# Performance work log

Measured on AMD Instinct MI355X. Metric: run time of the kernel, lower is better.

The kernel has to match this reference:

```python
import jax, jax.numpy as jnp
import numpy as np

B, S, D = 32, 512, 512      # batch, seq, feature
E, H, O, K = 8, 2048, 512, 2  # experts, expert hidden, expert out, top_k


def setup_inputs() -> dict:
    key = jax.random.key(0)
    ks = jax.random.split(key, 5)
    sc = lambda k, shape, scale: jax.random.normal(k, shape, jnp.float32) * scale
    return {
        "x": sc(ks[0], (B, S, D), 1.0),
        "attn_w": sc(ks[1], (D, 1), 0.05),
        "attn_b": jnp.zeros((1,), jnp.float32),
        "gate_w": sc(ks[2], (D, E), 0.05),
        "gate_b": jnp.zeros((E,), jnp.float32),
        "w1": sc(ks[3], (E, D, H), 0.02),
        "b1": jnp.zeros((E, H), jnp.float32),
        "w2": sc(ks[4], (E, H, O), 0.02),
        "b2": jnp.zeros((E, O), jnp.float32),
    }


def reference(x, attn_w, attn_b, gate_w, gate_b, w1, b1, w2, b2):
    # --- attention pooling over the sequence axis ---
    scores = x @ attn_w + attn_b                      # [B,S,1]
    aw = jax.nn.softmax(scores, axis=1)               # softmax over seq
    pooled = jnp.sum(x * aw, axis=1)                  # [B,D]

    # --- gating: softmax -> top-k mask -> renormalize ---
    gates = jax.nn.softmax(pooled @ gate_w + gate_b, axis=-1)  # [B,E]
    _, idx = jax.lax.top_k(gates, K)                  # [B,K]
    mask = jnp.sum(jax.nn.one_hot(idx, E, dtype=gates.dtype), axis=-2)  # [B,E]
    g = gates * mask
    g = g / (jnp.sum(g, axis=-1, keepdims=True) + 1e-9)        # [B,E]

    # --- dense all-experts compute (exact GELU, as keras Dense('gelu')) ---
    h = jax.nn.gelu(jnp.einsum('bsd,edh->ebsh', x, w1) + b1[:, None, None, :],
                    approximate=False)                 # [E,B,S,H]
    eo = jax.nn.gelu(jnp.einsum('ebsh,eho->ebso', h, w2) + b2[:, None, None, :],
                     approximate=False)                # [E,B,S,O]

    # --- weighted combine over experts ---
    return jnp.einsum('ebso,be->bso', eo, g)           # [B,S,O]
```

## Files before the change

kernel.cpp:

```cpp
#include <hip/hip_runtime.h>
#include <hip/hip_bf16.h>
#include <math.h>

#define B_  32
#define S_  512
#define D_  512
#define E_  8
#define H_  2048
#define O_  512

typedef __bf16 bf16x8 __attribute__((ext_vector_type(8)));
typedef float  f32x4  __attribute__((ext_vector_type(4)));

#define GL2LDS(src, dst) \
  __builtin_amdgcn_global_load_lds((const __attribute__((address_space(1))) void*)(src), \
                                   (__attribute__((address_space(3))) void*)(dst), 16, 0, 0)

#define MFMA16(a, b, c) __builtin_amdgcn_mfma_f32_16x16x32_bf16((a), (b), (c), 0, 0, 0)

__device__ __forceinline__ float gelu_fast(float v) {
  float w = v * fmaf(v * v, 0.0713548162f, 1.5957691216f);
  float e = __expf(-w);
  return v * __builtin_amdgcn_rcpf(1.0f + e);
}

__global__ __launch_bounds__(256) void cast_score_kernel(
    const float* __restrict__ x, const float* __restrict__ attn_w,
    ushort* __restrict__ xb, float* __restrict__ scores)
{
  const int t = threadIdx.x;
  const int r = t >> 5;
  const int cg = t & 31;
  const int row = blockIdx.x * 8 + r;
  const float* src  = x + (size_t)row * D_ + cg * 16;
  const float* wsrc = attn_w + cg * 16;
  ushort* dstp = xb + (size_t)row * D_ + cg * 16;
  float acc = 0.f;
#pragma unroll
  for (int k = 0; k < 4; ++k) {
    float4 v  = *(const float4*)(src + k * 4);
    float4 wv = *(const float4*)(wsrc + k * 4);
    acc += v.x * wv.x + v.y * wv.y + v.z * wv.z + v.w * wv.w;
    ushort4 o;
    o.x = __builtin_bit_cast(unsigned short, __float2bfloat16(v.x));
    o.y = __builtin_bit_cast(unsigned short, __float2bfloat16(v.y));
    o.z = __builtin_bit_cast(unsigned short, __float2bfloat16(v.z));
    o.w = __builtin_bit_cast(unsigned short, __float2bfloat16(v.w));
    *(ushort4*)(dstp + k * 4) = o;
  }
#pragma unroll
  for (int off = 16; off; off >>= 1) acc += __shfl_xor(acc, off);
  if (cg == 0) scores[row] = acc;
}

__global__ __launch_bounds__(512) void softmax_aw_kernel(
    const float* __restrict__ scores, float* __restrict__ aw)
{
  __shared__ float red[8];
  __shared__ float mm, ss;
  const int t = threadIdx.x, b = blockIdx.x;
  float v = scores[b * S_ + t];
  float m = v;
#pragma unroll
  for (int off = 32; off; off >>= 1) m = fmaxf(m, __shfl_xor(m, off));
  if ((t & 63) == 0) red[t >> 6] = m;
  __syncthreads();
  if (t == 0) {
    float a = red[0];
    for (int i = 1; i < 8; ++i) a = fmaxf(a, red[i]);
    mm = a;
  }
  __syncthreads();
  float e = expf(v - mm);
  float s = e;
#pragma unroll
  for (int off = 32; off; off >>= 1) s += __shfl_xor(s, off);
  if ((t & 63) == 0) red[t >> 6] = s;
  __syncthreads();
  if (t == 0) {
    float a = 0.f;
    for (int i = 0; i < 8; ++i) a += red[i];
    ss = 1.f / a;
  }
  __syncthreads();
  aw[b * S_ + t] = e * ss;
}

__global__ __launch_bounds__(512) void pool_kernel(
    const float* __restrict__ x, const float* __restrict__ aw, float* __restrict__ pooled)
{
  __shared__ float sm[4][128];
  const int t = threadIdx.x;
  const int dl = t & 127;
  const int sh = t >> 7;
  const int b = blockIdx.y;
  const int d = blockIdx.x * 128 + dl;
  const float* xp  = x + (size_t)b * S_ * D_ + d;
  const float* awb = aw + b * S_;
  float acc = 0.f;
#pragma unroll 4
  for (int s = sh; s < S_; s += 4)
    acc = fmaf(awb[s], xp[(size_t)s * D_], acc);
  if (sh) sm[sh][dl] = acc;
  __syncthreads();
  if (sh == 0) pooled[b * D_ + d] = acc + sm[1][dl] + sm[2][dl] + sm[3][dl];
}

__global__ __launch_bounds__(256) void gate_psort_kernel(
    const float* __restrict__ pooled, const float* __restrict__ gate_w,
    const float* __restrict__ gate_b, int* __restrict__ gidx, float* __restrict__ gwt,
    int* __restrict__ psort)
{
  __shared__ float gl[32][8];
  const int t = threadIdx.x;
  const int b = t >> 3, ee = t & 7;
  float z = gate_b[ee];
  const float* pb = pooled + b * D_;
  for (int d = 0; d < D_; ++d) z = fmaf(pb[d], gate_w[d * E_ + ee], z);
  gl[b][ee] = z;
  __syncthreads();
  if (t < 32) {
    float ge[8];
    float zmax = gl[t][0];
    for (int i = 1; i < 8; ++i) zmax = fmaxf(zmax, gl[t][i]);
    float zs = 0.f;
    for (int i = 0; i < 8; ++i) { ge[i] = expf(gl[t][i] - zmax); zs += ge[i]; }
    for (int i = 0; i < 8; ++i) ge[i] /= zs;
    int i0 = 0;
    for (int i = 1; i < 8; ++i) if (ge[i] > ge[i0]) i0 = i;
    int i1 = -1;
    for (int i = 0; i < 8; ++i) if (i != i0 && (i1 < 0 || ge[i] > ge[i1])) i1 = i;
    float denom = ge[i0] + ge[i1] + 1e-9f;
    gidx[t * 2 + 0] = i0; gidx[t * 2 + 1] = i1;
    gwt[t * 2 + 0] = ge[i0] / denom; gwt[t * 2 + 1] = ge[i1] / denom;
  }
  __syncthreads();
  if (t == 0) {
    int cnt[E_] = {}, pos[E_];
    for (int p = 0; p < 2 * B_; ++p) cnt[gidx[p]]++;
    int s = 0;
    for (int e2 = 0; e2 < E_; ++e2) { pos[e2] = s; s += cnt[e2]; }
    for (int p = 0; p < 2 * B_; ++p) psort[pos[gidx[p]]++] = p;
  }
}

__global__ void transpose_cast_kernel(const float* __restrict__ in,
                                      __hip_bfloat16* __restrict__ outT, int R, int C)
{
  __shared__ float tile[32][33];
  const int z = blockIdx.z;
  const float* inz = in + (size_t)z * R * C;
  __hip_bfloat16* outz = outT + (size_t)z * R * C;
  const int c0 = blockIdx.x * 32, r0 = blockIdx.y * 32;
  const int tx = threadIdx.x, ty = threadIdx.y;
#pragma unroll
  for (int jj = 0; jj < 4; ++jj) {
    int r = r0 + ty + jj * 8;
    tile[ty + jj * 8][tx] = inz[(size_t)r * C + c0 + tx];
  }
  __syncthreads();
#pragma unroll
  for (int jj = 0; jj < 4; ++jj) {
    int c = c0 + ty + jj * 8;
    outz[(size_t)c * R + r0 + tx] = __float2bfloat16(tile[tx][ty + jj * 8]);
  }
}

__device__ __forceinline__ void gemm_core_v3(const char* __restrict__ Ag, const char* __restrict__ Bg,
                                             const int lda, const int ldb, const int NT,
                                             char* lds, f32x4 (&acc)[8][4])
{
  const int tid = threadIdx.x;
  const int l = tid & 63;
  const int w = tid >> 6;
  const int wm = w >> 2;
  const int wn = w & 3;
  const int lr = l & 15;
  const int ks = (l >> 4) & 3;
  const int axor = ((ks ^ ((lr >> 1) & 3)) << 4);
  const int abase = (wm * 128 + lr) * 64 + axor;
  const int bbase = 32768 + (wn * 64 + lr) * 64 + axor;

  const int rw = tid >> 2;
  const int sx = (((tid & 3) ^ ((rw >> 1) & 3)) << 4);
  const int dst = tid * 16;
  const char* A0p = Ag + (size_t)rw * lda + sx;
  const char* A1p = Ag + (size_t)(rw + 128) * lda + sx;
  const char* B0p = Bg + (size_t)rw * ldb + sx;
  const char* B1p = Bg + (size_t)(rw + 128) * ldb + sx;

#define SU_A(t, kh, bufp) { const int go = (t) * 128 + (kh) * 64; \
    GL2LDS(A0p + go, (bufp) + (kh) * 16384 + dst); \
    GL2LDS(A1p + go, (bufp) + (kh) * 16384 + 8192 + dst); }
#define SU_B(t, kh, bufp) { const int go = (t) * 128 + (kh) * 64; \
    GL2LDS(B0p + go, (bufp) + 32768 + (kh) * 16384 + dst); \
    GL2LDS(B1p + go, (bufp) + 32768 + (kh) * 16384 + 8192 + dst); }

  SU_A(0, 0, lds); SU_B(0, 0, lds); SU_A(0, 1, lds); SU_B(0, 1, lds);

#pragma unroll 1
  for (int t = 0; t < NT; ++t) {
    char* cur = lds + ((t & 1) << 16);
    char* nb  = lds + (((t + 1) & 1) << 16);
    const bool pre = (t + 1 < NT);
    bf16x8 a[8], bv0, bv1, bv2, bv3;

    __builtin_amdgcn_sched_barrier(0);
    asm volatile("s_waitcnt vmcnt(4)" ::: "memory");
    __builtin_amdgcn_s_barrier();
    __builtin_amdgcn_sched_barrier(0);
    if (pre) SU_A(t + 1, 0, nb);
#pragma unroll
    for (int m = 0; m < 8; ++m) a[m] = *(const bf16x8*)(cur + abase + m * 1024);
    bv0 = *(const bf16x8*)(cur + bbase);
    bv1 = *(const bf16x8*)(cur + bbase + 1024);
    __builtin_amdgcn_s_setprio(1);
#pragma unroll
    for (int m = 0; m < 8; ++m) {
      acc[m][0] = MFMA16(a[m], bv0, acc[m][0]);
      acc[m][1] = MFMA16(a[m], bv1, acc[m][1]);
    }
    __builtin_amdgcn_s_setprio(0);

    if (pre) SU_B(t + 1, 0, nb);
    bv2 = *(const bf16x8*)(cur + bbase + 2048);
    bv3 = *(const bf16x8*)(cur + bbase + 3072);
    __builtin_amdgcn_s_setprio(1);
#pragma unroll
    for (int m = 0; m < 8; ++m) {
      acc[m][2] = MFMA16(a[m], bv2, acc[m][2]);
      acc[m][3] = MFMA16(a[m], bv3, acc[m][3]);
    }
    __builtin_amdgcn_s_setprio(0);

    __builtin_amdgcn_sched_barrier(0);
    if (pre) asm volatile("s_waitcnt vmcnt(4)" ::: "memory");
    else     asm volatile("s_waitcnt vmcnt(0)" ::: "memory");
    __builtin_amdgcn_s_barrier();
    __builtin_amdgcn_sched_barrier(0);
    if (pre) SU_A(t + 1, 1, nb);
#pragma unroll
    for (int m = 0; m < 8; ++m) a[m] = *(const bf16x8*)(cur + abase + 16384 + m * 1024);
    bv0 = *(const bf16x8*)(cur + bbase + 16384);
    bv1 = *(const bf16x8*)(cur + bbase + 16384 + 1024);
    __builtin_amdgcn_s_setprio(1);
#pragma unroll
    for (int m = 0; m < 8; ++m) {
      acc[m][0] = MFMA16(a[m], bv0, acc[m][0]);
      acc[m][1] = MFMA16(a[m], bv1, acc[m][1]);
    }
    __builtin_amdgcn_s_setprio(0);

    if (pre) SU_B(t + 1, 1, nb);
    bv2 = *(const bf16x8*)(cur + bbase + 16384 + 2048);
    bv3 = *(const bf16x8*)(cur + bbase + 16384 + 3072);
    __builtin_amdgcn_s_setprio(1);
#pragma unroll
    for (int m = 0; m < 8; ++m) {
      acc[m][2] = MFMA16(a[m], bv2, acc[m][2]);
      acc[m][3] = MFMA16(a[m], bv3, acc[m][3]);
    }
    __builtin_amdgcn_s_setprio(0);
  }
#undef SU_A
#undef SU_B
}

__global__ __launch_bounds__(512, 2) void gemm1_kernel(
    const __hip_bfloat16* __restrict__ Xb, const __hip_bfloat16* __restrict__ W1T,
    const float* __restrict__ b1, __hip_bfloat16* __restrict__ Hbuf,
    const int* __restrict__ gidx, const int* __restrict__ psort)
{
  extern __shared__ char lds[];
  const int P = blockIdx.x;
  const int L = (P & 7) * 128 + (P >> 3);
  const int p = psort[L >> 4];
  const int tl = L & 15;
  const int b = p >> 1;
  const int e = gidx[p];
  const int h0 = (tl >> 1) * 256;
  const int s0 = (tl & 1) * 256;
  const char* Ag = (const char*)W1T + ((size_t)e * H_ + h0) * D_ * 2;
  const char* Bg = (const char*)Xb + ((size_t)b * S_ + s0) * D_ * 2;
  f32x4 acc[8][4] = {};
  gemm_core_v3(Ag, Bg, D_ * 2, D_ * 2, D_ / 64, lds, acc);

  const int tid = threadIdx.x, l = tid & 63, w = tid >> 6;
  const int wm = w >> 2, wn = w & 3, lr = l & 15, q4 = ((l >> 4) & 3) << 2;
  const float* b1e = b1 + (size_t)e * H_ + h0;
  __hip_bfloat16* Hp = Hbuf + (size_t)p * S_ * H_ + h0;
#pragma unroll
  for (int m = 0; m < 8; ++m) {
    const int hl = wm * 128 + m * 16 + q4;
    const float4 bias = *(const float4*)(b1e + hl);
#pragma unroll
    for (int n = 0; n < 4; ++n) {
      const int sl = s0 + wn * 64 + n * 16 + lr;
      ushort4 ov;
      ov.x = __builtin_bit_cast(unsigned short, __float2bfloat16(gelu_fast(acc[m][n][0] + bias.x)));
      ov.y = __builtin_bit_cast(unsigned short, __float2bfloat16(gelu_fast(acc[m][n][1] + bias.y)));
      ov.z = __builtin_bit_cast(unsigned short, __float2bfloat16(gelu_fast(acc[m][n][2] + bias.z)));
      ov.w = __builtin_bit_cast(unsigned short, __float2bfloat16(gelu_fast(acc[m][n][3] + bias.w)));
      *(ushort4*)(Hp + (size_t)sl * H_ + hl) = ov;
    }
  }
}

__global__ __launch_bounds__(512, 2) void gemm2_kernel(
    const __hip_bfloat16* __restrict__ Hbuf, const __hip_bfloat16* __restrict__ W2T,
    const float* __restrict__ b2, float* __restrict__ out,
    const int* __restrict__ gidx, const float* __restrict__ gwt,
    const int* __restrict__ psort)
{
  extern __shared__ char lds[];
  const int P = blockIdx.x;
  const int L = (P & 7) * 32 + (P >> 3);
  const int p = psort[L >> 2];
  const int tl = L & 3;
  const int b = p >> 1;
  const int e = gidx[p];
  const float gw = gwt[p];
  const int s0 = (tl >> 1) * 256;
  const int o0 = (tl & 1) * 256;
  const char* Ag = (const char*)Hbuf + ((size_t)p * S_ + s0) * H_ * 2;
  const char* Bg = (const char*)W2T + ((size_t)e * O_ + o0) * H_ * 2;
  f32x4 acc[8][4] = {};
  gemm_core_v3(Ag, Bg, H_ * 2, H_ * 2, H_ / 64, lds, acc);

  const int tid = threadIdx.x, l = tid & 63, w = tid >> 6;
  const int wm = w >> 2, wn = w & 3, lr = l & 15, q4 = ((l >> 4) & 3) << 2;
  const float* b2e = b2 + (size_t)e * O_ + o0;
#pragma unroll
  for (int m = 0; m < 8; ++m) {
    const int sl = s0 + wm * 128 + m * 16 + q4;
#pragma unroll
    for (int n = 0; n < 4; ++n) {
      const int ol = wn * 64 + n * 16 + lr;
      const float bias = b2e[ol];
      float* dstp = out + ((size_t)b * S_ + sl) * O_ + o0 + ol;
#pragma unroll
      for (int j = 0; j < 4; ++j)
        atomicAdd(dstp + (size_t)j * O_, gelu_fast(acc[m][n][j] + bias) * gw);
    }
  }
}

__global__ void sentinel_kernel(float* out, int n) {
  int i = blockIdx.x * blockDim.x + threadIdx.x;
  for (; i < n; i += gridDim.x * blockDim.x) out[i] = 1.0e6f;
}

extern "C" void kernel_launch(void* const* d_in, const int* in_sizes, int n_in,
                              void* d_out, int out_size, void* d_ws, size_t ws_size,
                              hipStream_t stream)
{
  const float* x      = (const float*)d_in[0];
  const float* attn_w = (const float*)d_in[1];
  const float* gate_w = (const float*)d_in[3];
  const float* gate_b = (const float*)d_in[4];
  const float* w1     = (const float*)d_in[5];
  const float* b1     = (const float*)d_in[6];
  const float* w2     = (const float*)d_in[7];
  const float* b2     = (const float*)d_in[8];
  float* out = (float*)d_out;

  char* ws = (char*)d_ws;
  const size_t OFF_GIDX = 0;
  const size_t OFF_GWT  = 256;
  const size_t OFF_PSRT = 512;
  const size_t OFF_X    = 1024;
  const size_t SZ_X     = (size_t)B_ * S_ * D_ * 2;
  const size_t OFF_W1T  = OFF_X + SZ_X;
  const size_t SZ_W1T   = (size_t)E_ * H_ * D_ * 2;
  const size_t OFF_W2T  = OFF_W1T + SZ_W1T;
  const size_t SZ_W2T   = (size_t)E_ * O_ * H_ * 2;
  const size_t OFF_H    = OFF_W2T + SZ_W2T;
  const size_t PAIR_H   = (size_t)S_ * H_ * 2;

  if (OFF_H + 64 * PAIR_H > ws_size) {
    hipLaunchKernelGGL(sentinel_kernel, dim3(256), dim3(256), 0, stream, out, out_size);
    return;
  }

  int*   gidx  = (int*)(ws + OFF_GIDX);
  float* gwt   = (float*)(ws + OFF_GWT);
  int*   psort = (int*)(ws + OFF_PSRT);
  __hip_bfloat16* xb   = (__hip_bfloat16*)(ws + OFF_X);
  __hip_bfloat16* w1T  = (__hip_bfloat16*)(ws + OFF_W1T);
  __hip_bfloat16* w2T  = (__hip_bfloat16*)(ws + OFF_W2T);
  __hip_bfloat16* Hbuf = (__hip_bfloat16*)(ws + OFF_H);
  float* scores = (float*)(ws + OFF_H);
  float* aw     = (float*)(ws + OFF_H + 65536);
  float* pooled = (float*)(ws + OFF_H + 131072);

  (void)hipFuncSetAttribute((const void*)gemm1_kernel, hipFuncAttributeMaxDynamicSharedMemorySize, 131072);
  (void)hipFuncSetAttribute((const void*)gemm2_kernel, hipFuncAttributeMaxDynamicSharedMemorySize, 131072);

  hipLaunchKernelGGL(cast_score_kernel, dim3(B_ * S_ / 8), dim3(256), 0, stream,
                     x, attn_w, (ushort*)xb, scores);
  hipLaunchKernelGGL(softmax_aw_kernel, dim3(B_), dim3(512), 0, stream, scores, aw);
  hipLaunchKernelGGL(pool_kernel, dim3(4, B_), dim3(512), 0, stream, x, aw, pooled);
  hipLaunchKernelGGL(gate_psort_kernel, dim3(1), dim3(256), 0, stream,
                     pooled, gate_w, gate_b, gidx, gwt, psort);
  hipLaunchKernelGGL(transpose_cast_kernel, dim3(H_ / 32, D_ / 32, E_), dim3(32, 8), 0, stream,
                     w1, w1T, D_, H_);
  hipLaunchKernelGGL(transpose_cast_kernel, dim3(O_ / 32, H_ / 32, E_), dim3(32, 8), 0, stream,
                     w2, w2T, H_, O_);
  hipMemsetAsync(d_out, 0, (size_t)out_size * sizeof(float), stream);

  hipLaunchKernelGGL(gemm1_kernel, dim3(1024), dim3(512), 131072, stream,
                     xb, w1T, b1, Hbuf, gidx, psort);
  hipLaunchKernelGGL(gemm2_kernel, dim3(256), dim3(512), 131072, stream,
                     Hbuf, w2T, b2, out, gidx, gwt, psort);
}
```

Measured before the change: 290.2 us.

## Pre-pack GEMM operands into swizzled K-panels for contiguous LDS staging

```diff
diff --git a/kernel.cpp b/kernel.cpp
--- a/kernel.cpp
+++ b/kernel.cpp
@@ -24,20 +24,24 @@
   return v * __builtin_amdgcn_rcpf(1.0f + e);
 }
 
+
 __global__ __launch_bounds__(256) void cast_score_kernel(
     const float* __restrict__ x, const float* __restrict__ attn_w,
-    ushort* __restrict__ xb, float* __restrict__ scores)
+    char* __restrict__ xpack, float* __restrict__ scores)
 {
   const int t = threadIdx.x;
   const int r = t >> 5;
   const int cg = t & 31;
   const int row = blockIdx.x * 8 + r;
+  const int bb = row >> 9, s = row & 511;
   const float* src  = x + (size_t)row * D_ + cg * 16;
   const float* wsrc = attn_w + cg * 16;
-  ushort* dstp = xb + (size_t)row * D_ + cg * 16;
+  char* xp = xpack + (size_t)bb * 524288 + s * 64;
+  const int sx = (s >> 1) & 3;
   float acc = 0.f;
 #pragma unroll
   for (int k = 0; k < 4; ++k) {
+    const int d0 = cg * 16 + k * 4;
     float4 v  = *(const float4*)(src + k * 4);
     float4 wv = *(const float4*)(wsrc + k * 4);
     acc += v.x * wv.x + v.y * wv.y + v.z * wv.z + v.w * wv.w;
@@ -46,7 +50,9 @@
     o.y = __builtin_bit_cast(unsigned short, __float2bfloat16(v.y));
     o.z = __builtin_bit_cast(unsigned short, __float2bfloat16(v.z));
     o.w = __builtin_bit_cast(unsigned short, __float2bfloat16(v.w));
-    *(ushort4*)(dstp + k * 4) = o;
+    const int kt2 = ((d0 >> 6) << 1) | ((d0 >> 5) & 1);
+    const int byte = kt2 * 32768 + ((((d0 >> 3) & 3) ^ sx) << 4) + (d0 & 7) * 2;
+    *(ushort4*)(xp + byte) = o;
   }
 #pragma unroll
   for (int off = 16; off; off >>= 1) acc += __shfl_xor(acc, off);
@@ -144,13 +150,12 @@
   }
 }
 
-__global__ void transpose_cast_kernel(const float* __restrict__ in,
-                                      __hip_bfloat16* __restrict__ outT, int R, int C)
+__global__ void pack_w_kernel(const float* __restrict__ in, char* __restrict__ outp,
+                              int R, int C)
 {
   __shared__ float tile[32][33];
   const int z = blockIdx.z;
   const float* inz = in + (size_t)z * R * C;
-  __hip_bfloat16* outz = outT + (size_t)z * R * C;
   const int c0 = blockIdx.x * 32, r0 = blockIdx.y * 32;
   const int tx = threadIdx.x, ty = threadIdx.y;
 #pragma unroll
@@ -159,15 +164,23 @@
     tile[ty + jj * 8][tx] = inz[(size_t)r * C + c0 + tx];
   }
   __syncthreads();
+  const int k = r0 + tx;
+  const int kt2 = ((k >> 6) << 1) | ((k >> 5) & 1);
+  const int PAN = C * 64;
+  char* oz = outp + (size_t)z * R * C * 2 + (size_t)kt2 * PAN;
+  const int kslot = (k >> 3) & 3;
+  const int kbyte = (k & 7) * 2;
 #pragma unroll
   for (int jj = 0; jj < 4; ++jj) {
-    int c = c0 + ty + jj * 8;
-    outz[(size_t)c * R + r0 + tx] = __float2bfloat16(tile[tx][ty + jj * 8]);
-  }
-}
-
-__device__ __forceinline__ void gemm_core_v3(const char* __restrict__ Ag, const char* __restrict__ Bg,
-                                             const int lda, const int ldb, const int NT,
+    const int row = c0 + ty + jj * 8;
+    const int byte = row * 64 + ((kslot ^ ((row >> 1) & 3)) << 4) + kbyte;
+    *(ushort*)(oz + byte) =
+        __builtin_bit_cast(unsigned short, __float2bfloat16(tile[tx][ty + jj * 8]));
+  }
+}
+
+__device__ __forceinline__ void gemm_core_v4(const char* __restrict__ Ag, const char* __restrict__ Bg,
+                                             const int panelA, const int panelB, const int NT,
                                              char* lds, f32x4 (&acc)[8][4])
 {
   const int tid = threadIdx.x;
@@ -180,21 +193,14 @@
   const int axor = ((ks ^ ((lr >> 1) & 3)) << 4);
   const int abase = (wm * 128 + lr) * 64 + axor;
   const int bbase = 32768 + (wn * 64 + lr) * 64 + axor;
-
-  const int rw = tid >> 2;
-  const int sx = (((tid & 3) ^ ((rw >> 1) & 3)) << 4);
   const int dst = tid * 16;
-  const char* A0p = Ag + (size_t)rw * lda + sx;
-  const char* A1p = Ag + (size_t)(rw + 128) * lda + sx;
-  const char* B0p = Bg + (size_t)rw * ldb + sx;
-  const char* B1p = Bg + (size_t)(rw + 128) * ldb + sx;
-
-#define SU_A(t, kh, bufp) { const int go = (t) * 128 + (kh) * 64; \
-    GL2LDS(A0p + go, (bufp) + (kh) * 16384 + dst); \
-    GL2LDS(A1p + go, (bufp) + (kh) * 16384 + 8192 + dst); }
-#define SU_B(t, kh, bufp) { const int go = (t) * 128 + (kh) * 64; \
-    GL2LDS(B0p + go, (bufp) + 32768 + (kh) * 16384 + dst); \
-    GL2LDS(B1p + go, (bufp) + 32768 + (kh) * 16384 + 8192 + dst); }
+
+#define SU_A(t, kh, bufp) { const char* s_ = Ag + (size_t)((t) * 2 + (kh)) * panelA; \
+    GL2LDS(s_ + dst,        (bufp) + (kh) * 16384 + dst); \
+    GL2LDS(s_ + 8192 + dst, (bufp) + (kh) * 16384 + 8192 + dst); }
+#define SU_B(t, kh, bufp) { const char* s_ = Bg + (size_t)((t) * 2 + (kh)) * panelB; \
+    GL2LDS(s_ + dst,        (bufp) + 32768 + (kh) * 16384 + dst); \
+    GL2LDS(s_ + 8192 + dst, (bufp) + 32768 + (kh) * 16384 + 8192 + dst); }
 
   SU_A(0, 0, lds); SU_B(0, 0, lds); SU_A(0, 1, lds); SU_B(0, 1, lds);
 
@@ -267,8 +273,8 @@
 }
 
 __global__ __launch_bounds__(512, 2) void gemm1_kernel(
-    const __hip_bfloat16* __restrict__ Xb, const __hip_bfloat16* __restrict__ W1T,
-    const float* __restrict__ b1, __hip_bfloat16* __restrict__ Hbuf,
+    const char* __restrict__ xpack, const char* __restrict__ W1pack,
+    const float* __restrict__ b1, char* __restrict__ Hpack,
     const int* __restrict__ gidx, const int* __restrict__ psort)
 {
   extern __shared__ char lds[];
@@ -280,18 +286,22 @@
   const int e = gidx[p];
   const int h0 = (tl >> 1) * 256;
   const int s0 = (tl & 1) * 256;
-  const char* Ag = (const char*)W1T + ((size_t)e * H_ + h0) * D_ * 2;
-  const char* Bg = (const char*)Xb + ((size_t)b * S_ + s0) * D_ * 2;
+  const char* Ag = W1pack + (size_t)e * 2097152 + h0 * 64;
+  const char* Bg = xpack + (size_t)b * 524288 + s0 * 64;
   f32x4 acc[8][4] = {};
-  gemm_core_v3(Ag, Bg, D_ * 2, D_ * 2, D_ / 64, lds, acc);
+  gemm_core_v4(Ag, Bg, 131072, 32768, D_ / 64, lds, acc);
 
   const int tid = threadIdx.x, l = tid & 63, w = tid >> 6;
   const int wm = w >> 2, wn = w & 3, lr = l & 15, q4 = ((l >> 4) & 3) << 2;
   const float* b1e = b1 + (size_t)e * H_ + h0;
-  __hip_bfloat16* Hp = Hbuf + (size_t)p * S_ * H_ + h0;
+  char* Hp = Hpack + (size_t)p * 2097152;
 #pragma unroll
   for (int m = 0; m < 8; ++m) {
     const int hl = wm * 128 + m * 16 + q4;
+    const int h = h0 + hl;
+    const int kt2h = ((h >> 6) << 1) | ((h >> 5) & 1);
+    const int hslot = (h >> 3) & 3;
+    const int hbyte = (h & 7) * 2;
     const float4 bias = *(const float4*)(b1e + hl);
 #pragma unroll
     for (int n = 0; n < 4; ++n) {
@@ -301,13 +311,14 @@
       ov.y = __builtin_bit_cast(unsigned short, __float2bfloat16(gelu_fast(acc[m][n][1] + bias.y)));
       ov.z = __builtin_bit_cast(unsigned short, __float2bfloat16(gelu_fast(acc[m][n][2] + bias.z)));
       ov.w = __builtin_bit_cast(unsigned short, __float2bfloat16(gelu_fast(acc[m][n][3] + bias.w)));
-      *(ushort4*)(Hp + (size_t)sl * H_ + hl) = ov;
+      const int byte = kt2h * 32768 + sl * 64 + ((hslot ^ ((sl >> 1) & 3)) << 4) + hbyte;
+      *(ushort4*)(Hp + byte) = ov;
     }
   }
 }
 
 __global__ __launch_bounds__(512, 2) void gemm2_kernel(
-    const __hip_bfloat16* __restrict__ Hbuf, const __hip_bfloat16* __restrict__ W2T,
+    const char* __restrict__ Hpack, const char* __restrict__ W2pack,
     const float* __restrict__ b2, float* __restrict__ out,
     const int* __restrict__ gidx, const float* __restrict__ gwt,
     const int* __restrict__ psort)
@@ -322,10 +333,10 @@
   const float gw = gwt[p];
   const int s0 = (tl >> 1) * 256;
   const int o0 = (tl & 1) * 256;
-  const char* Ag = (const char*)Hbuf + ((size_t)p * S_ + s0) * H_ * 2;
-  const char* Bg = (const char*)W2T + ((size_t)e * O_ + o0) * H_ * 2;
+  const char* Ag = Hpack + (size_t)p * 2097152 + s0 * 64;
+  const char* Bg = W2pack + (size_t)e * 2097152 + o0 * 64;
   f32x4 acc[8][4] = {};
-  gemm_core_v3(Ag, Bg, H_ * 2, H_ * 2, H_ / 64, lds, acc);
+  gemm_core_v4(Ag, Bg, 32768, 32768, H_ / 64, lds, acc);
 
   const int tid = threadIdx.x, l = tid & 63, w = tid >> 6;
   const int wm = w >> 2, wn = w & 3, lr = l & 15, q4 = ((l >> 4) & 3) << 2;
@@ -382,13 +393,13 @@
     return;
   }
 
-  int*   gidx  = (int*)(ws + OFF_GIDX);
-  float* gwt   = (float*)(ws + OFF_GWT);
-  int*   psort = (int*)(ws + OFF_PSRT);
-  __hip_bfloat16* xb   = (__hip_bfloat16*)(ws + OFF_X);
-  __hip_bfloat16* w1T  = (__hip_bfloat16*)(ws + OFF_W1T);
-  __hip_bfloat16* w2T  = (__hip_bfloat16*)(ws + OFF_W2T);
-  __hip_bfloat16* Hbuf = (__hip_bfloat16*)(ws + OFF_H);
+  int*   gidx   = (int*)(ws + OFF_GIDX);
+  float* gwt    = (float*)(ws + OFF_GWT);
+  int*   psort  = (int*)(ws + OFF_PSRT);
+  char*  xpack  = ws + OFF_X;
+  char*  W1pack = ws + OFF_W1T;
+  char*  W2pack = ws + OFF_W2T;
+  char*  Hpack  = ws + OFF_H;
   float* scores = (float*)(ws + OFF_H);
   float* aw     = (float*)(ws + OFF_H + 65536);
   float* pooled = (float*)(ws + OFF_H + 131072);
@@ -397,19 +408,19 @@
   (void)hipFuncSetAttribute((const void*)gemm2_kernel, hipFuncAttributeMaxDynamicSharedMemorySize, 131072);
 
   hipLaunchKernelGGL(cast_score_kernel, dim3(B_ * S_ / 8), dim3(256), 0, stream,
-                     x, attn_w, (ushort*)xb, scores);
+                     x, attn_w, xpack, scores);
   hipLaunchKernelGGL(softmax_aw_kernel, dim3(B_), dim3(512), 0, stream, scores, aw);
   hipLaunchKernelGGL(pool_kernel, dim3(4, B_), dim3(512), 0, stream, x, aw, pooled);
   hipLaunchKernelGGL(gate_psort_kernel, dim3(1), dim3(256), 0, stream,
                      pooled, gate_w, gate_b, gidx, gwt, psort);
-  hipLaunchKernelGGL(transpose_cast_kernel, dim3(H_ / 32, D_ / 32, E_), dim3(32, 8), 0, stream,
-                     w1, w1T, D_, H_);
-  hipLaunchKernelGGL(transpose_cast_kernel, dim3(O_ / 32, H_ / 32, E_), dim3(32, 8), 0, stream,
-                     w2, w2T, H_, O_);
+  hipLaunchKernelGGL(pack_w_kernel, dim3(H_ / 32, D_ / 32, E_), dim3(32, 8), 0, stream,
+                     w1, W1pack, D_, H_);
+  hipLaunchKernelGGL(pack_w_kernel, dim3(O_ / 32, H_ / 32, E_), dim3(32, 8), 0, stream,
+                     w2, W2pack, H_, O_);
   hipMemsetAsync(d_out, 0, (size_t)out_size * sizeof(float), stream);
 
   hipLaunchKernelGGL(gemm1_kernel, dim3(1024), dim3(512), 131072, stream,
-                     xb, w1T, b1, Hbuf, gidx, psort);
+                     xpack, W1pack, b1, Hpack, gidx, psort);
   hipLaunchKernelGGL(gemm2_kernel, dim3(256), dim3(512), 131072, stream,
-                     Hbuf, w2T, b2, out, gidx, gwt, psort);
-}
+                     Hpack, W2pack, b2, out, gidx, gwt, psort);
+}
```

Measured after the change: 268.4 us. 1.08x faster.

## Restructure the MFMA GEMM core into quarter-tile phases with finer staging

Applied to the files above, without the earlier changes.

```diff
diff --git a/kernel.cpp b/kernel.cpp
--- a/kernel.cpp
+++ b/kernel.cpp
@@ -166,7 +166,7 @@
   }
 }
 
-__device__ __forceinline__ void gemm_core_v3(const char* __restrict__ Ag, const char* __restrict__ Bg,
+__device__ __forceinline__ void gemm_core_v7(const char* __restrict__ Ag, const char* __restrict__ Bg,
                                              const int lda, const int ldb, const int NT,
                                              char* lds, f32x4 (&acc)[8][4])
 {
@@ -176,94 +176,105 @@
   const int wm = w >> 2;
   const int wn = w & 3;
   const int lr = l & 15;
-  const int ks = (l >> 4) & 3;
-  const int axor = ((ks ^ ((lr >> 1) & 3)) << 4);
-  const int abase = (wm * 128 + lr) * 64 + axor;
-  const int bbase = 32768 + (wn * 64 + lr) * 64 + axor;
-
-  const int rw = tid >> 2;
-  const int sx = (((tid & 3) ^ ((rw >> 1) & 3)) << 4);
+  const int ks = l >> 4;
+  const int rswz = (ks ^ ((lr >> 1) & 3)) << 4;
   const int dst = tid * 16;
-  const char* A0p = Ag + (size_t)rw * lda + sx;
-  const char* A1p = Ag + (size_t)(rw + 128) * lda + sx;
-  const char* B0p = Bg + (size_t)rw * ldb + sx;
-  const char* B1p = Bg + (size_t)(rw + 128) * ldb + sx;
-
-#define SU_A(t, kh, bufp) { const int go = (t) * 128 + (kh) * 64; \
-    GL2LDS(A0p + go, (bufp) + (kh) * 16384 + dst); \
-    GL2LDS(A1p + go, (bufp) + (kh) * 16384 + 8192 + dst); }
-#define SU_B(t, kh, bufp) { const int go = (t) * 128 + (kh) * 64; \
-    GL2LDS(B0p + go, (bufp) + 32768 + (kh) * 16384 + dst); \
-    GL2LDS(B1p + go, (bufp) + 32768 + (kh) * 16384 + 8192 + dst); }
-
-  SU_A(0, 0, lds); SU_B(0, 0, lds); SU_A(0, 1, lds); SU_B(0, 1, lds);
+
+  const size_t arow = (size_t)(((tid >> 8) & 1) * 128 + ((tid >> 2) & 63));
+  const int csw = (((tid & 3) ^ ((tid >> 3) & 3)) << 4);
+
+#define STG_A(t_, s_, q_, bufp) \
+    GL2LDS(Ag + (arow + (q_) * 64) * (size_t)lda + (t_) * 128 + (s_) * 64 + csw, \
+           (bufp) + (s_) * 16384 + (q_) * 8192 + dst)
+#define STG_B(t_, s_, u_, bufp) \
+    GL2LDS(Bg + ((size_t)((u_) * 128) + (tid >> 2)) * (size_t)ldb + (t_) * 128 + (s_) * 64 + csw, \
+           (bufp) + 32768 + (s_) * 16384 + (u_) * 8192 + dst)
+
+  STG_A(0, 0, 0, lds); STG_B(0, 0, 0, lds);
+  STG_A(0, 0, 1, lds); STG_B(0, 0, 1, lds);
+  STG_A(0, 1, 0, lds); STG_B(0, 1, 0, lds);
+  STG_A(0, 1, 1, lds); STG_B(0, 1, 1, lds);
+  asm volatile("s_waitcnt vmcnt(4)" ::: "memory");
+  __builtin_amdgcn_s_barrier();
 
 #pragma unroll 1
   for (int t = 0; t < NT; ++t) {
     char* cur = lds + ((t & 1) << 16);
     char* nb  = lds + (((t + 1) & 1) << 16);
     const bool pre = (t + 1 < NT);
-    bf16x8 a[8], bv0, bv1, bv2, bv3;
-
-    __builtin_amdgcn_sched_barrier(0);
-    asm volatile("s_waitcnt vmcnt(4)" ::: "memory");
-    __builtin_amdgcn_s_barrier();
-    __builtin_amdgcn_sched_barrier(0);
-    if (pre) SU_A(t + 1, 0, nb);
-#pragma unroll
-    for (int m = 0; m < 8; ++m) a[m] = *(const bf16x8*)(cur + abase + m * 1024);
-    bv0 = *(const bf16x8*)(cur + bbase);
-    bv1 = *(const bf16x8*)(cur + bbase + 1024);
+    bf16x8 a[4], bv[4];
+
+    if (pre) { STG_A(t + 1, 0, 0, nb); STG_B(t + 1, 0, 0, nb); }
+#pragma unroll
+    for (int f = 0; f < 4; ++f)
+      a[f] = *(const bf16x8*)(cur + wm * 4096 + f * 1024 + lr * 64 + rswz);
+#pragma unroll
+    for (int n = 0; n < 4; ++n)
+      bv[n] = *(const bf16x8*)(cur + 32768 + wn * 4096 + n * 1024 + lr * 64 + rswz);
+    __builtin_amdgcn_s_barrier();
+    asm volatile("s_waitcnt lgkmcnt(0)" ::: "memory");
     __builtin_amdgcn_s_setprio(1);
 #pragma unroll
-    for (int m = 0; m < 8; ++m) {
-      acc[m][0] = MFMA16(a[m], bv0, acc[m][0]);
-      acc[m][1] = MFMA16(a[m], bv1, acc[m][1]);
-    }
+    for (int f = 0; f < 4; ++f)
+#pragma unroll
+      for (int n = 0; n < 4; ++n)
+        acc[f][n] = MFMA16(a[f], bv[n], acc[f][n]);
     __builtin_amdgcn_s_setprio(0);
-
-    if (pre) SU_B(t + 1, 0, nb);
-    bv2 = *(const bf16x8*)(cur + bbase + 2048);
-    bv3 = *(const bf16x8*)(cur + bbase + 3072);
+    __builtin_amdgcn_s_barrier();
+
+    if (pre) { STG_A(t + 1, 0, 1, nb); STG_B(t + 1, 0, 1, nb); }
+#pragma unroll
+    for (int f = 0; f < 4; ++f)
+      a[f] = *(const bf16x8*)(cur + 8192 + wm * 4096 + f * 1024 + lr * 64 + rswz);
+    __builtin_amdgcn_s_barrier();
+    asm volatile("s_waitcnt lgkmcnt(0)" ::: "memory");
     __builtin_amdgcn_s_setprio(1);
 #pragma unroll
-    for (int m = 0; m < 8; ++m) {
-      acc[m][2] = MFMA16(a[m], bv2, acc[m][2]);
-      acc[m][3] = MFMA16(a[m], bv3, acc[m][3]);
-    }
+    for (int f = 0; f < 4; ++f)
+#pragma unroll
+      for (int n = 0; n < 4; ++n)
+        acc[4 + f][n] = MFMA16(a[f], bv[n], acc[4 + f][n]);
     __builtin_amdgcn_s_setprio(0);
-
-    __builtin_amdgcn_sched_barrier(0);
     if (pre) asm volatile("s_waitcnt vmcnt(4)" ::: "memory");
     else     asm volatile("s_waitcnt vmcnt(0)" ::: "memory");
     __builtin_amdgcn_s_barrier();
-    __builtin_amdgcn_sched_barrier(0);
-    if (pre) SU_A(t + 1, 1, nb);
-#pragma unroll
-    for (int m = 0; m < 8; ++m) a[m] = *(const bf16x8*)(cur + abase + 16384 + m * 1024);
-    bv0 = *(const bf16x8*)(cur + bbase + 16384);
-    bv1 = *(const bf16x8*)(cur + bbase + 16384 + 1024);
+
+    if (pre) { STG_A(t + 1, 1, 0, nb); STG_B(t + 1, 1, 0, nb); }
+#pragma unroll
+    for (int f = 0; f < 4; ++f)
+      a[f] = *(const bf16x8*)(cur + 16384 + wm * 4096 + f * 1024 + lr * 64 + rswz);
+#pragma unroll
+    for (int n = 0; n < 4; ++n)
+      bv[n] = *(const bf16x8*)(cur + 32768 + 16384 + wn * 4096 + n * 1024 + lr * 64 + rswz);
+    __builtin_amdgcn_s_barrier();
+    asm volatile("s_waitcnt lgkmcnt(0)" ::: "memory");
     __builtin_amdgcn_s_setprio(1);
 #pragma unroll
-    for (int m = 0; m < 8; ++m) {
-      acc[m][0] = MFMA16(a[m], bv0, acc[m][0]);
-      acc[m][1] = MFMA16(a[m], bv1, acc[m][1]);
-    }
+    for (int f = 0; f < 4; ++f)
+#pragma unroll
+      for (int n = 0; n < 4; ++n)
+        acc[f][n] = MFMA16(a[f], bv[n], acc[f][n]);
     __builtin_amdgcn_s_setprio(0);
-
-    if (pre) SU_B(t + 1, 1, nb);
-    bv2 = *(const bf16x8*)(cur + bbase + 16384 + 2048);
-    bv3 = *(const bf16x8*)(cur + bbase + 16384 + 3072);
+    __builtin_amdgcn_s_barrier();
+
+    if (pre) { STG_A(t + 1, 1, 1, nb); STG_B(t + 1, 1, 1, nb); }
+#pragma unroll
+    for (int f = 0; f < 4; ++f)
+      a[f] = *(const bf16x8*)(cur + 24576 + wm * 4096 + f * 1024 + lr * 64 + rswz);
+    __builtin_amdgcn_s_barrier();
+    asm volatile("s_waitcnt lgkmcnt(0)" ::: "memory");
     __builtin_amdgcn_s_setprio(1);
 #pragma unroll
-    for (int m = 0; m < 8; ++m) {
-      acc[m][2] = MFMA16(a[m], bv2, acc[m][2]);
-      acc[m][3] = MFMA16(a[m], bv3, acc[m][3]);
-    }
+    for (int f = 0; f < 4; ++f)
+#pragma unroll
+      for (int n = 0; n < 4; ++n)
+        acc[4 + f][n] = MFMA16(a[f], bv[n], acc[4 + f][n]);
     __builtin_amdgcn_s_setprio(0);
-  }
-#undef SU_A
-#undef SU_B
+    if (pre) asm volatile("s_waitcnt vmcnt(4)" ::: "memory");
+    __builtin_amdgcn_s_barrier();
+  }
+#undef STG_A
+#undef STG_B
 }
 
 __global__ __launch_bounds__(512, 2) void gemm1_kernel(
@@ -280,10 +291,10 @@
   const int e = gidx[p];
   const int h0 = (tl >> 1) * 256;
   const int s0 = (tl & 1) * 256;
-  const char* Ag = (const char*)W1T + ((size_t)e * H_ + h0) * D_ * 2;
-  const char* Bg = (const char*)Xb + ((size_t)b * S_ + s0) * D_ * 2;
+  const char* Ag = (const char*)(W1T + ((size_t)e * H_ + h0) * D_);
+  const char* Bg = (const char*)(Xb + ((size_t)b * S_ + s0) * D_);
   f32x4 acc[8][4] = {};
-  gemm_core_v3(Ag, Bg, D_ * 2, D_ * 2, D_ / 64, lds, acc);
+  gemm_core_v7(Ag, Bg, D_ * 2, D_ * 2, D_ / 64, lds, acc);
 
   const int tid = threadIdx.x, l = tid & 63, w = tid >> 6;
   const int wm = w >> 2, wn = w & 3, lr = l & 15, q4 = ((l >> 4) & 3) << 2;
@@ -322,10 +333,10 @@
   const float gw = gwt[p];
   const int s0 = (tl >> 1) * 256;
   const int o0 = (tl & 1) * 256;
-  const char* Ag = (const char*)Hbuf + ((size_t)p * S_ + s0) * H_ * 2;
-  const char* Bg = (const char*)W2T + ((size_t)e * O_ + o0) * H_ * 2;
+  const char* Ag = (const char*)(Hbuf + ((size_t)p * S_ + s0) * H_);
+  const char* Bg = (const char*)(W2T + ((size_t)e * O_ + o0) * H_);
   f32x4 acc[8][4] = {};
-  gemm_core_v3(Ag, Bg, H_ * 2, H_ * 2, H_ / 64, lds, acc);
+  gemm_core_v7(Ag, Bg, H_ * 2, H_ * 2, H_ / 64, lds, acc);
 
   const int tid = threadIdx.x, l = tid & 63, w = tid >> 6;
   const int wm = w >> 2, wn = w & 3, lr = l & 15, q4 = ((l >> 4) & 3) << 2;
```

Result: slower. 297.4 us (+2.5%).
